# Optimization experiments

Hardware: AMD Instinct MI355X
Metric: run time of the kernel (lower is better)

## Reference

```python
import jax, jax.numpy as jnp
import numpy as np

HOPS = 3  # C[i].weight tied to A[i+1].weight -> HOPS+1 distinct tables E_0..E_HOPS


def setup_inputs() -> dict:
    key = jax.random.key(0)
    ks = jax.random.split(key, 10)
    B, M, K, E, G, V = 32, 2048, 4, 128, 128, 50000
    s = 1.0 / np.sqrt(E).astype(np.float32)
    context = jax.random.randint(ks[0], (B, M, K), 0, V)          # memory (triples)
    h_ = jax.random.normal(ks[1], (B, G), dtype=jnp.float32)      # prev GRU hidden
    y_ = jax.random.randint(ks[2], (B,), 0, V)                    # prev token
    emb = jax.random.normal(ks[3], (HOPS + 1, V, E), dtype=jnp.float32) * 0.1
    W_ih = jax.random.normal(ks[4], (3 * G, E), dtype=jnp.float32) * s
    W_hh = jax.random.normal(ks[5], (3 * G, G), dtype=jnp.float32) * s
    b_ih = jax.random.normal(ks[6], (3 * G,), dtype=jnp.float32) * s
    b_hh = jax.random.normal(ks[7], (3 * G,), dtype=jnp.float32) * s
    W_vocab = jax.random.normal(ks[8], (V, 2 * E), dtype=jnp.float32) * s
    b_vocab = jax.random.normal(ks[9], (V,), dtype=jnp.float32) * s
    return dict(context=context, h_=h_, y_=y_, emb=emb, W_ih=W_ih, W_hh=W_hh,
                b_ih=b_ih, b_hh=b_hh, W_vocab=W_vocab, b_vocab=b_vocab)


def gru_cell(x, h, W_ih, W_hh, b_ih, b_hh):
    # PyTorch GRU cell semantics (r, z, n gate order).
    gi = x @ W_ih.T + b_ih
    gh = h @ W_hh.T + b_hh
    i_r, i_z, i_n = jnp.split(gi, 3, axis=-1)
    h_r, h_z, h_n = jnp.split(gh, 3, axis=-1)
    r = jax.nn.sigmoid(i_r + h_r)
    z = jax.nn.sigmoid(i_z + h_z)
    n = jnp.tanh(i_n + r * h_n)
    return (1.0 - z) * n + z * h


def reference(context, h_, y_, emb, W_ih, W_hh, b_ih, b_hh, W_vocab, b_vocab):
    x = emb[0][y_]                                   # [B, E] A[0] embed of prev token
    h = gru_cell(x, h_, W_ih, W_hh, b_ih, b_hh)      # [B, G], G == E
    q = h
    o1 = None
    attn = None
    for hop in range(HOPS):
        mA = emb[hop][context].sum(axis=2)           # gather [B,M,K,E] -> sum over K -> [B,M,E]
        p = jnp.einsum('bme,be->bm', mA, q)          # attention scores over memory slots
        attn = jax.nn.softmax(p, axis=1)             # [B, M]
        mC = emb[hop + 1][context].sum(axis=2)       # C[hop] table (tied to A[hop+1])
        o = jnp.einsum('bm,bme->be', attn, mC)       # memory read [B, E]
        q = q + o
        if hop == 0:
            o1 = o
    logits = jnp.concatenate([h, o1], axis=1) @ W_vocab.T + b_vocab  # [B, V]
    p_vocab = jax.nn.softmax(logits, axis=1)
    return h, p_vocab, attn
```

## Files before the change

### kernel.cpp

```cpp
#include <hip/hip_runtime.h>
#include <math.h>

#define BB 32
#define MM 2048
#define KK 4
#define EE 128
#define GG 128
#define VV 50000
#define HOPS 3

__global__ __launch_bounds__(384) void gru_kernel(
    const float* __restrict__ emb0,
    const int*   __restrict__ y,
    const float* __restrict__ hprev,
    const float* __restrict__ W_ih,
    const float* __restrict__ W_hh,
    const float* __restrict__ b_ih,
    const float* __restrict__ b_hh,
    float* __restrict__ h_out,
    float* __restrict__ q,
    float* __restrict__ o1)
{
    int b = blockIdx.x;
    int t = threadIdx.x;
    __shared__ float x[EE], h[GG], gi[3*GG], gh[3*GG];
    if (t < EE)            x[t]       = emb0[(size_t)y[b]*EE + t];
    else if (t < 2*EE)     h[t-EE]    = hprev[b*GG + (t-EE)];
    if (t < EE) o1[b*EE + t] = 0.f;
    __syncthreads();
    {
        float accI = b_ih[t], accH = b_hh[t];
        const float* wi = W_ih + (size_t)t*EE;
        const float* wh = W_hh + (size_t)t*GG;
        #pragma unroll 8
        for (int e = 0; e < EE; e++) { accI += x[e]*wi[e]; accH += h[e]*wh[e]; }
        gi[t] = accI; gh[t] = accH;
    }
    __syncthreads();
    if (t < GG) {
        float r = 1.f/(1.f + __expf(-(gi[t]        + gh[t])));
        float z = 1.f/(1.f + __expf(-(gi[GG+t]     + gh[GG+t])));
        float n = tanhf(gi[2*GG+t] + r*gh[2*GG+t]);
        float hn = (1.f - z)*n + z*h[t];
        h_out[b*GG + t] = hn;
        q[b*GG + t]     = hn;
    }
}

__global__ __launch_bounds__(256) void t_kernel(
    const float* __restrict__ q,
    const float* __restrict__ embT,
    float* __restrict__ t)
{
    __shared__ float Ut[EE][32];
    __shared__ float Wt[32][132];
    int tid = threadIdx.x;
    for (int i = tid; i < EE*32; i += 256) {
        int e = i >> 5, b = i & 31;
        Ut[e][b] = q[b*EE + e];
    }
    int vg = tid & 31;
    int bg = tid >> 5;
    int v0 = blockIdx.x * 128;
    float acc[4][4];
    #pragma unroll
    for (int i = 0; i < 4; i++)
        #pragma unroll
        for (int j = 0; j < 4; j++) acc[i][j] = 0.f;

    int vrow = tid >> 1;
    int half = tid & 1;
    const float* wrow = embT + (size_t)(v0 + vrow)*EE + half*16;
    bool vok = (v0 + vrow) < VV;

    for (int ec = 0; ec < EE; ec += 32) {
        __syncthreads();
        #pragma unroll
        for (int j = 0; j < 4; j++) {
            float4 w = make_float4(0.f, 0.f, 0.f, 0.f);
            if (vok) w = *(const float4*)(wrow + ec + j*4);
            int e0 = half*16 + j*4;
            Wt[e0+0][vrow] = w.x;
            Wt[e0+1][vrow] = w.y;
            Wt[e0+2][vrow] = w.z;
            Wt[e0+3][vrow] = w.w;
        }
        __syncthreads();
        #pragma unroll 8
        for (int e = 0; e < 32; e++) {
            float4 w = *(const float4*)(&Wt[e][vg*4]);
            float4 u = *(const float4*)(&Ut[ec + e][bg*4]);
            acc[0][0] += w.x*u.x; acc[0][1] += w.x*u.y; acc[0][2] += w.x*u.z; acc[0][3] += w.x*u.w;
            acc[1][0] += w.y*u.x; acc[1][1] += w.y*u.y; acc[1][2] += w.y*u.z; acc[1][3] += w.y*u.w;
            acc[2][0] += w.z*u.x; acc[2][1] += w.z*u.y; acc[2][2] += w.z*u.z; acc[2][3] += w.z*u.w;
            acc[3][0] += w.w*u.x; acc[3][1] += w.w*u.y; acc[3][2] += w.w*u.z; acc[3][3] += w.w*u.w;
        }
    }
    #pragma unroll
    for (int i = 0; i < 4; i++) {
        int v = v0 + vg*4 + i;
        if (v < VV) {
            #pragma unroll
            for (int j = 0; j < 4; j++)
                t[(size_t)(bg*4 + j)*VV + v] = acc[i][j];
        }
    }
}

__global__ __launch_bounds__(256) void scores_lookup_kernel(
    const float* __restrict__ t,
    const int*   __restrict__ ctx,
    float* __restrict__ p)
{
    int gid = blockIdx.x*256 + threadIdx.x;
    int b   = gid >> 11;
    const int4 c = *(const int4*)(ctx + (size_t)gid*KK);
    const float* tb = t + (size_t)b*VV;
    p[gid] = tb[c.x] + tb[c.y] + tb[c.z] + tb[c.w];
}

template<int SAVE_O1>
__global__ __launch_bounds__(256) void oacc_gather_kernel(
    const float* __restrict__ embT,
    const int*   __restrict__ ctx,
    const float* __restrict__ p,
    float* __restrict__ q,
    float* __restrict__ o1)
{
    int blk = blockIdx.x;
    int b = blk >> 5, s = blk & 31;
    int t = threadIdx.x;
    int w = t >> 6, lane = t & 63;

    const float* row = p + (size_t)b*MM;
    float v[8];
    float mx = -INFINITY;
    #pragma unroll
    for (int i = 0; i < 8; i++) { v[i] = row[t + i*256]; mx = fmaxf(mx, v[i]); }
    __shared__ float red[6];
    #pragma unroll
    for (int off = 32; off; off >>= 1) mx = fmaxf(mx, __shfl_down(mx, off));
    if (lane == 0) red[w] = mx;
    __syncthreads();
    if (t == 0) red[4] = fmaxf(fmaxf(red[0],red[1]), fmaxf(red[2],red[3]));
    __syncthreads();
    mx = red[4];
    float sum = 0.f;
    #pragma unroll
    for (int i = 0; i < 8; i++) sum += __expf(v[i] - mx);
    #pragma unroll
    for (int off = 32; off; off >>= 1) sum += __shfl_down(sum, off);
    __syncthreads();
    if (lane == 0) red[w] = sum;
    __syncthreads();
    if (t == 0) red[5] = 1.f / (red[0]+red[1]+red[2]+red[3]);
    __syncthreads();
    float rs = red[5];

    int m0 = s*64 + w*16;
    float ax = 0.f, ay = 0.f;
    for (int i = 0; i < 16; i++) {
        int m = m0 + i;
        float a = __expf(row[m] - mx) * rs;
        const int4 c = *(const int4*)(ctx + (size_t)(b*MM + m)*KK);
        float2 v0 = *(const float2*)(embT + (size_t)c.x*EE + lane*2);
        float2 v1 = *(const float2*)(embT + (size_t)c.y*EE + lane*2);
        float2 v2 = *(const float2*)(embT + (size_t)c.z*EE + lane*2);
        float2 v3 = *(const float2*)(embT + (size_t)c.w*EE + lane*2);
        ax += a * (v0.x + v1.x + v2.x + v3.x);
        ay += a * (v0.y + v1.y + v2.y + v3.y);
    }
    __shared__ float acc_red[4][EE];
    acc_red[w][lane*2]   = ax;
    acc_red[w][lane*2+1] = ay;
    __syncthreads();
    if (t < EE) {
        float vv = acc_red[0][t] + acc_red[1][t] + acc_red[2][t] + acc_red[3][t];
        atomicAdd(&q[b*EE + t], vv);
        if (SAVE_O1) atomicAdd(&o1[b*EE + t], vv);
    }
}

__global__ __launch_bounds__(1024) void attn_fused_kernel(
    const float* __restrict__ t,
    const int*   __restrict__ ctx,
    float* __restrict__ attn_out)
{
    int b   = blockIdx.x;
    int tid = threadIdx.x;
    const float* tb = t + (size_t)b*VV;
    int m1 = tid, m2 = tid + 1024;
    const int4 c1 = *(const int4*)(ctx + ((size_t)b*MM + m1)*KK);
    const int4 c2 = *(const int4*)(ctx + ((size_t)b*MM + m2)*KK);
    float s1 = tb[c1.x] + tb[c1.y] + tb[c1.z] + tb[c1.w];
    float s2 = tb[c2.x] + tb[c2.y] + tb[c2.z] + tb[c2.w];

    __shared__ float red[16];
    __shared__ float redm, reds;
    int wv = tid >> 6, lane = tid & 63;

    float mx = fmaxf(s1, s2);
    #pragma unroll
    for (int off = 32; off; off >>= 1) mx = fmaxf(mx, __shfl_down(mx, off));
    if (lane == 0) red[wv] = mx;
    __syncthreads();
    if (tid == 0) {
        float m = red[0];
        #pragma unroll
        for (int i = 1; i < 16; i++) m = fmaxf(m, red[i]);
        redm = m;
    }
    __syncthreads();
    mx = redm;
    float e1 = __expf(s1 - mx), e2 = __expf(s2 - mx);
    float sum = e1 + e2;
    #pragma unroll
    for (int off = 32; off; off >>= 1) sum += __shfl_down(sum, off);
    __syncthreads();
    if (lane == 0) red[wv] = sum;
    __syncthreads();
    if (tid == 0) {
        float s = 0.f;
        #pragma unroll
        for (int i = 0; i < 16; i++) s += red[i];
        reds = 1.f / s;
    }
    __syncthreads();
    float rs = reds;
    attn_out[(size_t)b*MM + m1] = e1 * rs;
    attn_out[(size_t)b*MM + m2] = e2 * rs;
}

__global__ __launch_bounds__(256) void logits_kernel(
    const float* __restrict__ h,
    const float* __restrict__ o1,
    const float* __restrict__ Wv,
    const float* __restrict__ bv,
    float* __restrict__ logits)
{
    __shared__ float Ut[256][32];
    __shared__ float Wt[32][132];
    int t = threadIdx.x;
    for (int i = t; i < 256*32; i += 256) {
        int e = i >> 5, b = i & 31;
        Ut[e][b] = (e < GG) ? h[b*GG + e] : o1[b*EE + (e - GG)];
    }
    int vg = t & 31;
    int bg = t >> 5;
    int v0 = blockIdx.x * 128;
    float acc[4][4];
    #pragma unroll
    for (int i = 0; i < 4; i++)
        #pragma unroll
        for (int j = 0; j < 4; j++) acc[i][j] = 0.f;

    int vrow = t >> 1;
    int half = t & 1;
    const float* wrow = Wv + (size_t)(v0 + vrow)*256 + half*16;
    bool vok = (v0 + vrow) < VV;

    for (int ec = 0; ec < 256; ec += 32) {
        __syncthreads();
        #pragma unroll
        for (int j = 0; j < 4; j++) {
            float4 w = make_float4(0.f, 0.f, 0.f, 0.f);
            if (vok) w = *(const float4*)(wrow + ec + j*4);
            int e0 = half*16 + j*4;
            Wt[e0+0][vrow] = w.x;
            Wt[e0+1][vrow] = w.y;
            Wt[e0+2][vrow] = w.z;
            Wt[e0+3][vrow] = w.w;
        }
        __syncthreads();
        #pragma unroll 8
        for (int e = 0; e < 32; e++) {
            float4 w = *(const float4*)(&Wt[e][vg*4]);
            float4 u = *(const float4*)(&Ut[ec + e][bg*4]);
            acc[0][0] += w.x*u.x; acc[0][1] += w.x*u.y; acc[0][2] += w.x*u.z; acc[0][3] += w.x*u.w;
            acc[1][0] += w.y*u.x; acc[1][1] += w.y*u.y; acc[1][2] += w.y*u.z; acc[1][3] += w.y*u.w;
            acc[2][0] += w.z*u.x; acc[2][1] += w.z*u.y; acc[2][2] += w.z*u.z; acc[2][3] += w.z*u.w;
            acc[3][0] += w.w*u.x; acc[3][1] += w.w*u.y; acc[3][2] += w.w*u.z; acc[3][3] += w.w*u.w;
        }
    }
    #pragma unroll
    for (int i = 0; i < 4; i++) {
        int v = v0 + vg*4 + i;
        if (v < VV) {
            float bb = bv[v];
            #pragma unroll
            for (int j = 0; j < 4; j++)
                logits[(size_t)(bg*4 + j)*VV + v] = acc[i][j] + bb;
        }
    }
}

#define VCHUNK 6250
__global__ __launch_bounds__(256) void vpart_kernel(
    const float* __restrict__ logits,
    float* __restrict__ part)
{
    int blk = blockIdx.x;
    int b = blk >> 3, c = blk & 7;
    int t = threadIdx.x;
    const float* row = logits + (size_t)b*VV;
    int start = c*VCHUNK;
    int end   = min(start + VCHUNK, VV);
    __shared__ float red[4];
    int w = t >> 6, lane = t & 63;
    float mx = -INFINITY;
    for (int i = start + t; i < end; i += 256) mx = fmaxf(mx, row[i]);
    #pragma unroll
    for (int off = 32; off; off >>= 1) mx = fmaxf(mx, __shfl_down(mx, off));
    if (lane == 0) red[w] = mx;
    __syncthreads();
    float m = fmaxf(fmaxf(red[0], red[1]), fmaxf(red[2], red[3]));
    float sum = 0.f;
    for (int i = start + t; i < end; i += 256) sum += __expf(row[i] - m);
    #pragma unroll
    for (int off = 32; off; off >>= 1) sum += __shfl_down(sum, off);
    __syncthreads();
    if (lane == 0) red[w] = sum;
    __syncthreads();
    if (t == 0) {
        part[blk*2]   = m;
        part[blk*2+1] = red[0] + red[1] + red[2] + red[3];
    }
}

__global__ __launch_bounds__(256) void vfinal_kernel(
    float* __restrict__ logits,
    const float* __restrict__ part)
{
    int i = blockIdx.x*256 + threadIdx.x;
    if (i >= BB*VV) return;
    int b = i / VV;
    const float* pp = part + b*16;
    float M = -INFINITY;
    #pragma unroll
    for (int c = 0; c < 8; c++) M = fmaxf(M, pp[c*2]);
    float S = 0.f;
    #pragma unroll
    for (int c = 0; c < 8; c++) S += pp[c*2+1] * __expf(pp[c*2] - M);
    logits[i] = __expf(logits[i] - M) * (1.f / S);
}

extern "C" void kernel_launch(void* const* d_in, const int* in_sizes, int n_in,
                              void* d_out, int out_size, void* d_ws, size_t ws_size,
                              hipStream_t stream) {
    const int*   ctx    = (const int*)  d_in[0];
    const float* h_prev = (const float*)d_in[1];
    const int*   y      = (const int*)  d_in[2];
    const float* emb    = (const float*)d_in[3];
    const float* W_ih   = (const float*)d_in[4];
    const float* W_hh   = (const float*)d_in[5];
    const float* b_ih   = (const float*)d_in[6];
    const float* b_hh   = (const float*)d_in[7];
    const float* Wv     = (const float*)d_in[8];
    const float* bv     = (const float*)d_in[9];

    float* out_h    = (float*)d_out;
    float* out_pv   = out_h + BB*GG;
    float* out_attn = out_pv + (size_t)BB*VV;

    float* ws   = (float*)d_ws;
    float* q    = ws;
    float* o1   = q + BB*EE;
    float* p    = o1 + BB*EE;
    float* t    = p + BB*MM;
    float* part = t + (size_t)BB*VV;

    const float* e0 = emb;
    const float* e1 = emb + (size_t)1*VV*EE;
    const float* e2 = emb + (size_t)2*VV*EE;

    gru_kernel<<<BB, 384, 0, stream>>>(emb, y, h_prev, W_ih, W_hh, b_ih, b_hh, out_h, q, o1);

    t_kernel<<<391, 256, 0, stream>>>(q, e0, t);
    scores_lookup_kernel<<<(BB*MM)/256, 256, 0, stream>>>(t, ctx, p);
    oacc_gather_kernel<1><<<BB*32, 256, 0, stream>>>(e1, ctx, p, q, o1);

    t_kernel<<<391, 256, 0, stream>>>(q, e1, t);
    scores_lookup_kernel<<<(BB*MM)/256, 256, 0, stream>>>(t, ctx, p);
    oacc_gather_kernel<0><<<BB*32, 256, 0, stream>>>(e2, ctx, p, q, nullptr);

    t_kernel<<<391, 256, 0, stream>>>(q, e2, t);
    attn_fused_kernel<<<BB, 1024, 0, stream>>>(t, ctx, out_attn);

    logits_kernel<<<391, 256, 0, stream>>>(out_h, o1, Wv, bv, out_pv);
    vpart_kernel<<<BB*8, 256, 0, stream>>>(out_pv, part);
    vfinal_kernel<<<(BB*VV + 255)/256, 256, 0, stream>>>(out_pv, part);
}
```

Measured before the change: 339.0 us.

## Fuse score lookup into attention-read kernel and single-kernel vocab softmax

Removes the separate scores_lookup kernel. Each oacc block now recomputes all 2048 scores for its batch row from the t buffer and ctx, keeping them in shared memory. This is 32x redundant gather work per batch, traded against one kernel launch and the p round trip. It also replaces the two-kernel vocab softmax (partials plus a final pass) with one 1024-thread block per batch row that does max, sum and normalise in place, using only 32 blocks.

```diff
diff --git a/kernel.cpp b/kernel.cpp
--- a/kernel.cpp
+++ b/kernel.cpp
@@ -7,7 +7,6 @@
 #define EE 128
 #define GG 128
 #define VV 50000
-#define HOPS 3
 
 __global__ __launch_bounds__(384) void gru_kernel(
     const float* __restrict__ emb0,
@@ -107,42 +106,42 @@
     }
 }
 
-__global__ __launch_bounds__(256) void scores_lookup_kernel(
-    const float* __restrict__ t,
+template<int SAVE_O1>
+__global__ __launch_bounds__(256) void oaccL_kernel(
+    const float* __restrict__ embC,
     const int*   __restrict__ ctx,
-    float* __restrict__ p)
-{
-    int gid = blockIdx.x*256 + threadIdx.x;
-    int b   = gid >> 11;
-    const int4 c = *(const int4*)(ctx + (size_t)gid*KK);
-    const float* tb = t + (size_t)b*VV;
-    p[gid] = tb[c.x] + tb[c.y] + tb[c.z] + tb[c.w];
-}
-
-template<int SAVE_O1>
-__global__ __launch_bounds__(256) void oacc_gather_kernel(
-    const float* __restrict__ embT,
-    const int*   __restrict__ ctx,
-    const float* __restrict__ p,
+    const float* __restrict__ tbuf,
     float* __restrict__ q,
     float* __restrict__ o1)
 {
     int blk = blockIdx.x;
     int b = blk >> 5, s = blk & 31;
-    int t = threadIdx.x;
-    int w = t >> 6, lane = t & 63;
-
-    const float* row = p + (size_t)b*MM;
+    int tid = threadIdx.x;
+    int w = tid >> 6, lane = tid & 63;
+
+    __shared__ float psh[MM];
+    __shared__ float red[6];
+    __shared__ float accr[4][EE];
+
+    const float* tb = tbuf + (size_t)b*VV;
+    const int*   cb = ctx + (size_t)b*MM*KK;
+
     float v[8];
     float mx = -INFINITY;
     #pragma unroll
-    for (int i = 0; i < 8; i++) { v[i] = row[t + i*256]; mx = fmaxf(mx, v[i]); }
-    __shared__ float red[6];
+    for (int i = 0; i < 8; i++) {
+        int m = tid + i*256;
+        const int4 c = *(const int4*)(cb + (size_t)m*KK);
+        float sc = tb[c.x] + tb[c.y] + tb[c.z] + tb[c.w];
+        psh[m] = sc;
+        v[i] = sc;
+        mx = fmaxf(mx, sc);
+    }
     #pragma unroll
     for (int off = 32; off; off >>= 1) mx = fmaxf(mx, __shfl_down(mx, off));
     if (lane == 0) red[w] = mx;
     __syncthreads();
-    if (t == 0) red[4] = fmaxf(fmaxf(red[0],red[1]), fmaxf(red[2],red[3]));
+    if (tid == 0) red[4] = fmaxf(fmaxf(red[0],red[1]), fmaxf(red[2],red[3]));
     __syncthreads();
     mx = red[4];
     float sum = 0.f;
@@ -153,31 +152,32 @@
     __syncthreads();
     if (lane == 0) red[w] = sum;
     __syncthreads();
-    if (t == 0) red[5] = 1.f / (red[0]+red[1]+red[2]+red[3]);
+    if (tid == 0) red[5] = 1.f / (red[0]+red[1]+red[2]+red[3]);
     __syncthreads();
     float rs = red[5];
 
     int m0 = s*64 + w*16;
     float ax = 0.f, ay = 0.f;
+    #pragma unroll 2
     for (int i = 0; i < 16; i++) {
         int m = m0 + i;
-        float a = __expf(row[m] - mx) * rs;
-        const int4 c = *(const int4*)(ctx + (size_t)(b*MM + m)*KK);
-        float2 v0 = *(const float2*)(embT + (size_t)c.x*EE + lane*2);
-        float2 v1 = *(const float2*)(embT + (size_t)c.y*EE + lane*2);
-        float2 v2 = *(const float2*)(embT + (size_t)c.z*EE + lane*2);
-        float2 v3 = *(const float2*)(embT + (size_t)c.w*EE + lane*2);
+        float a = __expf(psh[m] - mx) * rs;
+        const int4 c = *(const int4*)(cb + (size_t)m*KK);
+        float2 v0 = *(const float2*)(embC + (size_t)c.x*EE + lane*2);
+        float2 v1 = *(const float2*)(embC + (size_t)c.y*EE + lane*2);
+        float2 v2 = *(const float2*)(embC + (size_t)c.z*EE + lane*2);
+        float2 v3 = *(const float2*)(embC + (size_t)c.w*EE + lane*2);
         ax += a * (v0.x + v1.x + v2.x + v3.x);
         ay += a * (v0.y + v1.y + v2.y + v3.y);
     }
-    __shared__ float acc_red[4][EE];
-    acc_red[w][lane*2]   = ax;
-    acc_red[w][lane*2+1] = ay;
-    __syncthreads();
-    if (t < EE) {
-        float vv = acc_red[0][t] + acc_red[1][t] + acc_red[2][t] + acc_red[3][t];
-        atomicAdd(&q[b*EE + t], vv);
-        if (SAVE_O1) atomicAdd(&o1[b*EE + t], vv);
+    __syncthreads();
+    accr[w][lane*2]   = ax;
+    accr[w][lane*2+1] = ay;
+    __syncthreads();
+    if (tid < EE) {
+        float vv = accr[0][tid] + accr[1][tid] + accr[2][tid] + accr[3][tid];
+        atomicAdd(&q[b*EE + tid], vv);
+        if (SAVE_O1) atomicAdd(&o1[b*EE + tid], vv);
     }
 }
 
@@ -294,54 +294,45 @@
     }
 }
 
-#define VCHUNK 6250
-__global__ __launch_bounds__(256) void vpart_kernel(
-    const float* __restrict__ logits,
-    float* __restrict__ part)
-{
-    int blk = blockIdx.x;
-    int b = blk >> 3, c = blk & 7;
-    int t = threadIdx.x;
-    const float* row = logits + (size_t)b*VV;
-    int start = c*VCHUNK;
-    int end   = min(start + VCHUNK, VV);
-    __shared__ float red[4];
-    int w = t >> 6, lane = t & 63;
+__global__ __launch_bounds__(1024) void vsm_kernel(
+    float* __restrict__ logits)
+{
+    int b = blockIdx.x, tid = threadIdx.x;
+    float* row = logits + (size_t)b*VV;
+    __shared__ float red[16];
+    __shared__ float redm, reds;
+    int w = tid >> 6, lane = tid & 63;
+
     float mx = -INFINITY;
-    for (int i = start + t; i < end; i += 256) mx = fmaxf(mx, row[i]);
+    for (int i = tid; i < VV; i += 1024) mx = fmaxf(mx, row[i]);
     #pragma unroll
     for (int off = 32; off; off >>= 1) mx = fmaxf(mx, __shfl_down(mx, off));
     if (lane == 0) red[w] = mx;
     __syncthreads();
-    float m = fmaxf(fmaxf(red[0], red[1]), fmaxf(red[2], red[3]));
-    float sum = 0.f;
-    for (int i = start + t; i < end; i += 256) sum += __expf(row[i] - m);
-    #pragma unroll
-    for (int off = 32; off; off >>= 1) sum += __shfl_down(sum, off);
-    __syncthreads();
-    if (lane == 0) red[w] = sum;
-    __syncthreads();
-    if (t == 0) {
-        part[blk*2]   = m;
-        part[blk*2+1] = red[0] + red[1] + red[2] + red[3];
-    }
-}
-
-__global__ __launch_bounds__(256) void vfinal_kernel(
-    float* __restrict__ logits,
-    const float* __restrict__ part)
-{
-    int i = blockIdx.x*256 + threadIdx.x;
-    if (i >= BB*VV) return;
-    int b = i / VV;
-    const float* pp = part + b*16;
-    float M = -INFINITY;
-    #pragma unroll
-    for (int c = 0; c < 8; c++) M = fmaxf(M, pp[c*2]);
-    float S = 0.f;
-    #pragma unroll
-    for (int c = 0; c < 8; c++) S += pp[c*2+1] * __expf(pp[c*2] - M);
-    logits[i] = __expf(logits[i] - M) * (1.f / S);
+    if (tid == 0) {
+        float m = red[0];
+        #pragma unroll
+        for (int i = 1; i < 16; i++) m = fmaxf(m, red[i]);
+        redm = m;
+    }
+    __syncthreads();
+    float M = redm;
+    float s = 0.f;
+    for (int i = tid; i < VV; i += 1024) s += __expf(row[i] - M);
+    #pragma unroll
+    for (int off = 32; off; off >>= 1) s += __shfl_down(s, off);
+    __syncthreads();
+    if (lane == 0) red[w] = s;
+    __syncthreads();
+    if (tid == 0) {
+        float z = 0.f;
+        #pragma unroll
+        for (int i = 0; i < 16; i++) z += red[i];
+        reds = 1.f / z;
+    }
+    __syncthreads();
+    float invS = reds;
+    for (int i = tid; i < VV; i += 1024) row[i] = __expf(row[i] - M) * invS;
 }
 
 extern "C" void kernel_launch(void* const* d_in, const int* in_sizes, int n_in,
@@ -365,9 +356,7 @@
     float* ws   = (float*)d_ws;
     float* q    = ws;
     float* o1   = q + BB*EE;
-    float* p    = o1 + BB*EE;
-    float* t    = p + BB*MM;
-    float* part = t + (size_t)BB*VV;
+    float* tbuf = o1 + BB*EE;
 
     const float* e0 = emb;
     const float* e1 = emb + (size_t)1*VV*EE;
@@ -375,18 +364,15 @@
 
     gru_kernel<<<BB, 384, 0, stream>>>(emb, y, h_prev, W_ih, W_hh, b_ih, b_hh, out_h, q, o1);
 
-    t_kernel<<<391, 256, 0, stream>>>(q, e0, t);
-    scores_lookup_kernel<<<(BB*MM)/256, 256, 0, stream>>>(t, ctx, p);
-    oacc_gather_kernel<1><<<BB*32, 256, 0, stream>>>(e1, ctx, p, q, o1);
-
-    t_kernel<<<391, 256, 0, stream>>>(q, e1, t);
-    scores_lookup_kernel<<<(BB*MM)/256, 256, 0, stream>>>(t, ctx, p);
-    oacc_gather_kernel<0><<<BB*32, 256, 0, stream>>>(e2, ctx, p, q, nullptr);
-
-    t_kernel<<<391, 256, 0, stream>>>(q, e2, t);
-    attn_fused_kernel<<<BB, 1024, 0, stream>>>(t, ctx, out_attn);
+    t_kernel<<<391, 256, 0, stream>>>(q, e0, tbuf);
+    oaccL_kernel<1><<<BB*32, 256, 0, stream>>>(e1, ctx, tbuf, q, o1);
+
+    t_kernel<<<391, 256, 0, stream>>>(q, e1, tbuf);
+    oaccL_kernel<0><<<BB*32, 256, 0, stream>>>(e2, ctx, tbuf, q, nullptr);
+
+    t_kernel<<<391, 256, 0, stream>>>(q, e2, tbuf);
+    attn_fused_kernel<<<BB, 1024, 0, stream>>>(tbuf, ctx, out_attn);
 
     logits_kernel<<<391, 256, 0, stream>>>(out_h, o1, Wv, bv, out_pv);
-    vpart_kernel<<<BB*8, 256, 0, stream>>>(out_pv, part);
-    vfinal_kernel<<<(BB*VV + 255)/256, 256, 0, stream>>>(out_pv, part);
-}
+    vsm_kernel<<<BB, 1024, 0, stream>>>(out_pv);
+}
```

New measurement: 395.7 us. 16.7% more time.

## Reuse summed memory rows from gather pass instead of full-vocab projection for later hops

Applied to the files above, without the earlier changes.

The gather pass that sums the embedding rows for the memory read now also writes the per-slot summed vectors (B×M×E) to a workspace buffer. The next hop computes its attention scores as a dot product of those stored rows with q, replacing the V-sized table projection (t_kernel) plus index lookup for hops 1 and 2. The final softmax becomes a standalone per-batch kernel. This avoids two passes over a 50000×128 embedding table and a 32×V intermediate, at the cost of writing and then reading two 32 MB buffers.

```diff
diff --git a/kernel.cpp b/kernel.cpp
--- a/kernel.cpp
+++ b/kernel.cpp
@@ -7,7 +7,6 @@
 #define EE 128
 #define GG 128
 #define VV 50000
-#define HOPS 3
 
 __global__ __launch_bounds__(384) void gru_kernel(
     const float* __restrict__ emb0,
@@ -120,10 +119,11 @@
 }
 
 template<int SAVE_O1>
-__global__ __launch_bounds__(256) void oacc_gather_kernel(
+__global__ __launch_bounds__(256) void oacc_fused_kernel(
     const float* __restrict__ embT,
     const int*   __restrict__ ctx,
     const float* __restrict__ p,
+    float* __restrict__ S_out,
     float* __restrict__ q,
     float* __restrict__ o1)
 {
@@ -167,8 +167,11 @@
         float2 v1 = *(const float2*)(embT + (size_t)c.y*EE + lane*2);
         float2 v2 = *(const float2*)(embT + (size_t)c.z*EE + lane*2);
         float2 v3 = *(const float2*)(embT + (size_t)c.w*EE + lane*2);
-        ax += a * (v0.x + v1.x + v2.x + v3.x);
-        ay += a * (v0.y + v1.y + v2.y + v3.y);
+        float sx = v0.x + v1.x + v2.x + v3.x;
+        float sy = v0.y + v1.y + v2.y + v3.y;
+        *(float2*)(S_out + ((size_t)b*MM + m)*EE + lane*2) = make_float2(sx, sy);
+        ax += a * sx;
+        ay += a * sy;
     }
     __shared__ float acc_red[4][EE];
     acc_red[w][lane*2]   = ax;
@@ -181,54 +184,53 @@
     }
 }
 
-__global__ __launch_bounds__(1024) void attn_fused_kernel(
-    const float* __restrict__ t,
-    const int*   __restrict__ ctx,
-    float* __restrict__ attn_out)
-{
-    int b   = blockIdx.x;
-    int tid = threadIdx.x;
-    const float* tb = t + (size_t)b*VV;
-    int m1 = tid, m2 = tid + 1024;
-    const int4 c1 = *(const int4*)(ctx + ((size_t)b*MM + m1)*KK);
-    const int4 c2 = *(const int4*)(ctx + ((size_t)b*MM + m2)*KK);
-    float s1 = tb[c1.x] + tb[c1.y] + tb[c1.z] + tb[c1.w];
-    float s2 = tb[c2.x] + tb[c2.y] + tb[c2.z] + tb[c2.w];
-
-    __shared__ float red[16];
-    __shared__ float redm, reds;
-    int wv = tid >> 6, lane = tid & 63;
-
-    float mx = fmaxf(s1, s2);
+__global__ __launch_bounds__(256) void scores_s_kernel(
+    const float* __restrict__ S,
+    const float* __restrict__ q,
+    float* __restrict__ p)
+{
+    int gid  = blockIdx.x * 4 + (threadIdx.x >> 6);
+    int lane = threadIdx.x & 63;
+    int b    = gid >> 11;
+    float2 sv = *(const float2*)(S + (size_t)gid*EE + lane*2);
+    float2 qv = *(const float2*)(q + b*EE + lane*2);
+    float acc = sv.x*qv.x + sv.y*qv.y;
+    #pragma unroll
+    for (int off = 32; off; off >>= 1) acc += __shfl_down(acc, off);
+    if (lane == 0) p[gid] = acc;
+}
+
+__global__ __launch_bounds__(256) void softmax_m_kernel(
+    const float* __restrict__ p,
+    float* __restrict__ attn)
+{
+    int b = blockIdx.x, t = threadIdx.x;
+    const float* row = p + (size_t)b*MM;
+    float v[8];
+    float mx = -INFINITY;
+    #pragma unroll
+    for (int i = 0; i < 8; i++) { v[i] = row[t + i*256]; mx = fmaxf(mx, v[i]); }
+    __shared__ float red[6];
+    int w = t >> 6, lane = t & 63;
     #pragma unroll
     for (int off = 32; off; off >>= 1) mx = fmaxf(mx, __shfl_down(mx, off));
-    if (lane == 0) red[wv] = mx;
-    __syncthreads();
-    if (tid == 0) {
-        float m = red[0];
-        #pragma unroll
-        for (int i = 1; i < 16; i++) m = fmaxf(m, red[i]);
-        redm = m;
-    }
-    __syncthreads();
-    mx = redm;
-    float e1 = __expf(s1 - mx), e2 = __expf(s2 - mx);
-    float sum = e1 + e2;
+    if (lane == 0) red[w] = mx;
+    __syncthreads();
+    if (t == 0) { float m2 = fmaxf(fmaxf(red[0],red[1]), fmaxf(red[2],red[3])); red[4] = m2; }
+    __syncthreads();
+    mx = red[4];
+    float sum = 0.f;
+    #pragma unroll
+    for (int i = 0; i < 8; i++) { v[i] = __expf(v[i] - mx); sum += v[i]; }
     #pragma unroll
     for (int off = 32; off; off >>= 1) sum += __shfl_down(sum, off);
-    __syncthreads();
-    if (lane == 0) red[wv] = sum;
-    __syncthreads();
-    if (tid == 0) {
-        float s = 0.f;
-        #pragma unroll
-        for (int i = 0; i < 16; i++) s += red[i];
-        reds = 1.f / s;
-    }
-    __syncthreads();
-    float rs = reds;
-    attn_out[(size_t)b*MM + m1] = e1 * rs;
-    attn_out[(size_t)b*MM + m2] = e2 * rs;
+    if (lane == 0) red[w] = sum;
+    __syncthreads();
+    if (t == 0) { red[5] = 1.f / (red[0]+red[1]+red[2]+red[3]); }
+    __syncthreads();
+    float rs = red[5];
+    #pragma unroll
+    for (int i = 0; i < 8; i++) attn[(size_t)b*MM + t + i*256] = v[i]*rs;
 }
 
 __global__ __launch_bounds__(256) void logits_kernel(
@@ -366,8 +368,10 @@
     float* q    = ws;
     float* o1   = q + BB*EE;
     float* p    = o1 + BB*EE;
-    float* t    = p + BB*MM;
-    float* part = t + (size_t)BB*VV;
+    float* tbuf = p + BB*MM;
+    float* S1   = tbuf + (size_t)BB*VV;
+    float* S2   = S1 + (size_t)BB*MM*EE;
+    float* part = S2 + (size_t)BB*MM*EE;
 
     const float* e0 = emb;
     const float* e1 = emb + (size_t)1*VV*EE;
@@ -375,16 +379,15 @@
 
     gru_kernel<<<BB, 384, 0, stream>>>(emb, y, h_prev, W_ih, W_hh, b_ih, b_hh, out_h, q, o1);
 
-    t_kernel<<<391, 256, 0, stream>>>(q, e0, t);
-    scores_lookup_kernel<<<(BB*MM)/256, 256, 0, stream>>>(t, ctx, p);
-    oacc_gather_kernel<1><<<BB*32, 256, 0, stream>>>(e1, ctx, p, q, o1);
-
-    t_kernel<<<391, 256, 0, stream>>>(q, e1, t);
-    scores_lookup_kernel<<<(BB*MM)/256, 256, 0, stream>>>(t, ctx, p);
-    oacc_gather_kernel<0><<<BB*32, 256, 0, stream>>>(e2, ctx, p, q, nullptr);
-
-    t_kernel<<<391, 256, 0, stream>>>(q, e2, t);
-    attn_fused_kernel<<<BB, 1024, 0, stream>>>(t, ctx, out_attn);
+    t_kernel<<<391, 256, 0, stream>>>(q, e0, tbuf);
+    scores_lookup_kernel<<<(BB*MM)/256, 256, 0, stream>>>(tbuf, ctx, p);
+    oacc_fused_kernel<1><<<BB*32, 256, 0, stream>>>(e1, ctx, p, S1, q, o1);
+
+    scores_s_kernel<<<(BB*MM)/4, 256, 0, stream>>>(S1, q, p);
+    oacc_fused_kernel<0><<<BB*32, 256, 0, stream>>>(e2, ctx, p, S2, q, nullptr);
+
+    scores_s_kernel<<<(BB*MM)/4, 256, 0, stream>>>(S2, q, p);
+    softmax_m_kernel<<<BB, 256, 0, stream>>>(p, out_attn);
 
     logits_kernel<<<391, 256, 0, stream>>>(out_h, o1, Wv, bv, out_pv);
     vpart_kernel<<<BB*8, 256, 0, stream>>>(out_pv, part);
```

Result: faster. 320.4 us (-5.5%).
